# Kernel tuning notes

Measured on AMD Instinct MI355X. Metric: run time of the kernel, lower is better.

The kernel has to match this reference:

```python
import jax, jax.numpy as jnp
import numpy as np

N = 8192
IN_F = 512
OUT_F = 128
ALPHA = 0.2  # leaky relu negative slope
NEG_BIG = -1e10
RND_SCALE = 1e5


def setup_inputs() -> dict:
    key = jax.random.key(0)
    k1, k2, k3, k4, k5 = jax.random.split(key, 5)
    h = jax.random.normal(k1, (N, IN_F), dtype=jnp.float32)
    adj = jax.random.randint(k2, (N, N), 0, 2, dtype=jnp.int32)
    W = jax.random.normal(k3, (IN_F, OUT_F), dtype=jnp.float32) * 0.05
    a = jax.random.normal(k4, (2 * OUT_F, 1), dtype=jnp.float32) * 0.1
    # rnd in original is 1e5*(rand-0.5); same distribution here
    rnd = RND_SCALE * (jax.random.uniform(k5, (N, OUT_F), dtype=jnp.float32) - 0.5)
    return {"h": h, "adj": adj, "W": W, "a": a, "rnd": rnd}


def reference(h, adj, W, a, rnd):
    Wh = h @ W                              # [N, OUT_F]
    Wh1 = Wh @ a[:OUT_F, :]                 # [N, 1]
    Wh2 = Wh @ a[OUT_F:, :]                 # [N, 1]
    e = jax.nn.leaky_relu(Wh1 + Wh2.T, negative_slope=ALPHA)  # [N, N]
    attention = jnp.where(adj > 0, e, NEG_BIG)
    attention = jax.nn.softmax(attention, axis=1)
    h_prime = attention @ Wh                # [N, OUT_F]
    h_prime = (h_prime + rnd) / RND_SCALE
    return jax.nn.elu(h_prime)
```

## Files before the change

kernel.cpp:

```cpp
#include <hip/hip_runtime.h>

#define N 8192
#define IN_F 512
#define OUT_F 128
#define NW (N / 8)
#define SPLITK 8
#define KC 1024
#define LOG2E 1.4426950408889634f
#define LN2 0.6931471805599453f

typedef __attribute__((ext_vector_type(4))) float f32x4;
typedef __attribute__((ext_vector_type(8))) short bf16x8;
typedef __attribute__((ext_vector_type(8))) unsigned short u16x8;

__device__ __forceinline__ short f2bf(float f) {
    union { float f; unsigned u; } c; c.f = f;
    unsigned r = c.u + 0x7FFFu + ((c.u >> 16) & 1u);
    return (short)(r >> 16);
}

__device__ __forceinline__ float exp2fast(float x) {
#if __has_builtin(__builtin_amdgcn_exp2f)
    return __builtin_amdgcn_exp2f(x);
#else
    return __expf(x * LN2);
#endif
}

__device__ __forceinline__ void load_lds16(const void* g, void* l) {
    __builtin_amdgcn_global_load_lds((const __attribute__((address_space(1))) unsigned*)g,
                                     (__attribute__((address_space(3))) unsigned*)l,
                                     16, 0, 0);
}

__global__ __launch_bounds__(256) void conv_W(const float* __restrict__ W, short* __restrict__ WT) {
    int idx = blockIdx.x * 256 + threadIdx.x;
    int n = idx & (OUT_F - 1);
    int k = idx >> 7;
    WT[(size_t)n * IN_F + k] = f2bf(W[idx]);
}

__global__ __launch_bounds__(256) void mkmask(const int* __restrict__ adj,
                                              unsigned char* __restrict__ maskR) {
    const int wave = threadIdx.x >> 6, lane = threadIdx.x & 63;
    const size_t m = (size_t)blockIdx.x * 4 + wave;
    const int4* ap = (const int4*)(adj + m * N);
    unsigned char* mp = maskR + m * NW;
#pragma unroll 4
    for (int it = 0; it < 16; it++) {
        int b4 = it * 128 + lane * 2;
        int4 a0 = ap[b4], a1 = ap[b4 + 1];
        unsigned b = (unsigned)(a0.x > 0) | ((unsigned)(a0.y > 0) << 1) |
                     ((unsigned)(a0.z > 0) << 2) | ((unsigned)(a0.w > 0) << 3) |
                     ((unsigned)(a1.x > 0) << 4) | ((unsigned)(a1.y > 0) << 5) |
                     ((unsigned)(a1.z > 0) << 6) | ((unsigned)(a1.w > 0) << 7);
        mp[it * 64 + lane] = (unsigned char)b;
    }
}

__global__ __launch_bounds__(256) void gemm_hW(const float* __restrict__ h,
                                               const short* __restrict__ WT,
                                               const float* __restrict__ a,
                                               short* __restrict__ WhT,
                                               float* __restrict__ sOut,
                                               float* __restrict__ tOut) {
    const int tid = threadIdx.x;
    const int wave = tid >> 6, lane = tid & 63;
    const int row16 = lane & 15, kgrp = lane >> 4;
    const int m0 = blockIdx.x * 16;
    const int kbase = wave * 128;

    f32x4 acc[8] = {};
    const float4* hp = (const float4*)(h + (size_t)(m0 + row16) * IN_F + kbase);

#pragma unroll
    for (int kk = 0; kk < 128; kk += 32) {
        float4 u0 = hp[kk / 4 + kgrp * 2];
        float4 u1 = hp[kk / 4 + kgrp * 2 + 1];
        bf16x8 af;
        af[0] = f2bf(u0.x); af[1] = f2bf(u0.y); af[2] = f2bf(u0.z); af[3] = f2bf(u0.w);
        af[4] = f2bf(u1.x); af[5] = f2bf(u1.y); af[6] = f2bf(u1.z); af[7] = f2bf(u1.w);
#pragma unroll
        for (int nt = 0; nt < 8; nt++) {
            bf16x8 bf_ = *(const bf16x8*)(WT + (size_t)(nt * 16 + row16) * IN_F + kbase + kk + kgrp * 8);
            acc[nt] = __builtin_amdgcn_mfma_f32_16x16x32_bf16(af, bf_, acc[nt], 0, 0, 0);
        }
    }

    __shared__ float red[4][16][132];
#pragma unroll
    for (int nt = 0; nt < 8; nt++)
#pragma unroll
        for (int r = 0; r < 4; r++)
            red[wave][kgrp * 4 + r][nt * 16 + row16] = acc[nt][r];
    __syncthreads();

    const int row = tid >> 4, seg = tid & 15;
    float v[8];
#pragma unroll
    for (int e = 0; e < 8; e++) {
        int c = seg * 8 + e;
        v[e] = red[0][row][c] + red[1][row][c] + red[2][row][c] + red[3][row][c];
    }
    float sp = 0.f, tp = 0.f;
#pragma unroll
    for (int e = 0; e < 8; e++) {
        sp += v[e] * a[seg * 8 + e];
        tp += v[e] * a[OUT_F + seg * 8 + e];
    }
    sp += __shfl_xor(sp, 1); tp += __shfl_xor(tp, 1);
    sp += __shfl_xor(sp, 2); tp += __shfl_xor(tp, 2);
    sp += __shfl_xor(sp, 4); tp += __shfl_xor(tp, 4);
    sp += __shfl_xor(sp, 8); tp += __shfl_xor(tp, 8);
    if (seg == 0) {
        sOut[m0 + row] = sp * LOG2E;
        tOut[m0 + row] = tp * LOG2E;
    }
#pragma unroll
    for (int e = 0; e < 8; e++)
        WhT[(size_t)(seg * 8 + e) * N + m0 + row] = f2bf(v[e]);
}

__global__ __launch_bounds__(256, 4) void attn(const unsigned char* __restrict__ maskR,
                                               const short* __restrict__ WhT,
                                               const float* __restrict__ s,
                                               const float* __restrict__ t,
                                               unsigned short* __restrict__ num,
                                               float* __restrict__ lpart) {
    const int tid = threadIdx.x;
    const int wave = tid >> 6, lane = tid & 63;
    const int row16 = lane & 15, kgrp = lane >> 4;
    const int m0 = blockIdx.x * 64 + wave * 16;
    const int m  = m0 + row16;
    const int ks = blockIdx.y * KC;

    __shared__ short Bs[2][2][128 * 32];
    __shared__ float tl[KC];

    for (int i = tid; i < KC; i += 256) tl[i] = t[ks + i];

    const float s_m = s[m];
    const int4* mp = (const int4*)(maskR + (size_t)m * NW + (ks >> 3));
    int4 mcur = mp[0], mnxt = mp[1];

    auto stageB = [&](int sup, int par) {
        const int k0 = ks + sup * 64;
#pragma unroll
        for (int d = 0; d < 2; d++)
#pragma unroll
            for (int q = 0; q < 2; q++) {
                int nrow = wave * 32 + q * 16 + (lane >> 2);
                const short* g = WhT + (size_t)nrow * N + k0 + d * 32 + (lane & 3) * 8;
                load_lds16(g, &Bs[par][d][(wave * 32 + q * 16) * 32]);
            }
    };

    f32x4 acc[8] = {};
    float lsum = 0.f;

    stageB(0, 0);
    __syncthreads();

    for (int sp2 = 0; sp2 < 8; sp2++) {
#pragma unroll
        for (int ss = 0; ss < 2; ss++) {
            const int sp = sp2 * 2 + ss;
            const int par = sp & 1;
            if (sp + 1 < 16) stageB(sp + 1, par ^ 1);
#pragma unroll
            for (int d = 0; d < 2; d++) {
                const int g = sp * 2 + d;
                const unsigned dw = (unsigned)((const int*)&mcur)[ss * 2 + d];
                const unsigned mbyte = (dw >> (kgrp * 8)) & 0xFFu;

                const float* tp = tl + g * 32 + kgrp * 8;
                float4 tA = *(const float4*)tp;
                float4 tB = *(const float4*)(tp + 4);
                float tv[8] = { tA.x, tA.y, tA.z, tA.w, tB.x, tB.y, tB.z, tB.w };

                bf16x8 bfr[8];
                const short* base = &Bs[par][d][0];
#pragma unroll
                for (int ni = 0; ni < 8; ni++)
                    bfr[ni] = *(const bf16x8*)(base + (ni * 16 + row16) * 32 + kgrp * 8);

                unsigned pu[8];
#pragma unroll
                for (int e = 0; e < 8; e++) {
                    float x = s_m + tv[e];
                    x = fmaxf(x, 0.2f * x);
                    float p = exp2fast(x);
                    unsigned u = __float_as_uint(p) & 0xFFFF0000u;
                    u = ((mbyte >> e) & 1u) ? u : 0u;
                    lsum += __uint_as_float(u);
                    pu[e] = u;
                }
                bf16x8 af;
                unsigned* au = (unsigned*)&af;
#pragma unroll
                for (int q = 0; q < 4; q++) au[q] = (pu[2 * q] >> 16) | pu[2 * q + 1];
#pragma unroll
                for (int ni = 0; ni < 8; ni++)
                    acc[ni] = __builtin_amdgcn_mfma_f32_16x16x32_bf16(af, bfr[ni], acc[ni], 0, 0, 0);
            }
            __syncthreads();
        }
        mcur = mnxt;
        if (sp2 + 2 < 8) mnxt = mp[sp2 + 2];
    }

    {
        float v = lsum;
        v += __shfl_xor(v, 16);
        v += __shfl_xor(v, 32);
        if (kgrp == 0) lpart[(size_t)blockIdx.y * N + m] = v;
    }

    unsigned short* np_ = num + ((size_t)blockIdx.y * N + m0) * OUT_F;
#pragma unroll
    for (int ni = 0; ni < 8; ni++) {
        int n = ni * 16 + row16;
#pragma unroll
        for (int r = 0; r < 4; r++)
            np_[(size_t)(kgrp * 4 + r) * OUT_F + n] = (unsigned short)f2bf(acc[ni][r]);
    }
}

__global__ __launch_bounds__(256) void finalize(const unsigned short* __restrict__ num,
                                                const float* __restrict__ lpart,
                                                const float* __restrict__ rnd,
                                                float* __restrict__ out) {
    int idx = blockIdx.x * 256 + threadIdx.x;
    int m = idx >> 4;
    int c = (idx & 15) * 8;
    size_t g = (size_t)m * OUT_F + c;

    float nm[8] = {};
#pragma unroll
    for (int bk = 0; bk < SPLITK; bk++) {
        u16x8 v = *(const u16x8*)(num + (size_t)bk * N * OUT_F + g);
#pragma unroll
        for (int e = 0; e < 8; e++) nm[e] += __uint_as_float((unsigned)v[e] << 16);
    }
    float l = 0.f;
#pragma unroll
    for (int bk = 0; bk < SPLITK; bk++) l += lpart[(size_t)bk * N + m];
    float inv = 1.f / fmaxf(l, 1e-30f);

    float4 r0 = *(const float4*)(rnd + g);
    float4 r1 = *(const float4*)(rnd + g + 4);
    float rv[8] = { r0.x, r0.y, r0.z, r0.w, r1.x, r1.y, r1.z, r1.w };
    float ov[8];
#pragma unroll
    for (int e = 0; e < 8; e++) {
        float x = (nm[e] * inv + rv[e]) * 1e-5f;
        ov[e] = x > 0.f ? x : __expf(x) - 1.f;
    }
    *(float4*)(out + g)     = make_float4(ov[0], ov[1], ov[2], ov[3]);
    *(float4*)(out + g + 4) = make_float4(ov[4], ov[5], ov[6], ov[7]);
}

extern "C" void kernel_launch(void* const* d_in, const int* in_sizes, int n_in,
                              void* d_out, int out_size, void* d_ws, size_t ws_size,
                              hipStream_t stream) {
    const float* h   = (const float*)d_in[0];
    const int*   adj = (const int*)d_in[1];
    const float* W   = (const float*)d_in[2];
    const float* a   = (const float*)d_in[3];
    const float* rnd = (const float*)d_in[4];
    float* out = (float*)d_out;

    char* w = (char*)d_ws;
    short* WT    = (short*)(w);
    short* WhT   = (short*)(w + 131072);
    float* sv    = (float*)(w + 2228224);
    float* tv    = (float*)(w + 2260992);
    float* lpart = (float*)(w + 2293760);
    unsigned char* maskR = (unsigned char*)(w + 2555904);
    unsigned short* num  = (unsigned short*)(w + 10944512);

    conv_W  <<<256, 256, 0, stream>>>(W, WT);
    mkmask  <<<2048, 256, 0, stream>>>(adj, maskR);
    gemm_hW <<<512, 256, 0, stream>>>(h, WT, a, WhT, sv, tv);
    attn    <<<dim3(128, SPLITK), 256, 0, stream>>>(maskR, WhT, sv, tv, num, lpart);
    finalize<<<(N * OUT_F / 8) / 256, 256, 0, stream>>>(num, lpart, rnd, out);
}
```

Before: 427.3 us.

## Fuse adjacency mask construction into attention kernel, dropping separate bitmask pass

The separate mkmask kernel is removed. The attention kernel now streams int32 adjacency tiles straight from global memory into registers, prefetched one step ahead, and converts them to byte masks in per-wave LDS. Each lane then reads its 8 mask bytes as a 64-bit word. The t vector is read from global memory each step instead of being cached in LDS. This avoids the extra kernel launch and the maskR write and re-read. In exchange the attn kernel carries the full 256MB adjacency read inside its main loop, which adds register and memory pressure there.

Result: slower. 437.8 us (+2.4%).

```diff
diff --git a/kernel.cpp b/kernel.cpp
--- a/kernel.cpp
+++ b/kernel.cpp
@@ -3,7 +3,6 @@
 #define N 8192
 #define IN_F 512
 #define OUT_F 128
-#define NW (N / 8)
 #define SPLITK 8
 #define KC 1024
 #define LOG2E 1.4426950408889634f
@@ -38,24 +37,6 @@
     int n = idx & (OUT_F - 1);
     int k = idx >> 7;
     WT[(size_t)n * IN_F + k] = f2bf(W[idx]);
-}
-
-__global__ __launch_bounds__(256) void mkmask(const int* __restrict__ adj,
-                                              unsigned char* __restrict__ maskR) {
-    const int wave = threadIdx.x >> 6, lane = threadIdx.x & 63;
-    const size_t m = (size_t)blockIdx.x * 4 + wave;
-    const int4* ap = (const int4*)(adj + m * N);
-    unsigned char* mp = maskR + m * NW;
-#pragma unroll 4
-    for (int it = 0; it < 16; it++) {
-        int b4 = it * 128 + lane * 2;
-        int4 a0 = ap[b4], a1 = ap[b4 + 1];
-        unsigned b = (unsigned)(a0.x > 0) | ((unsigned)(a0.y > 0) << 1) |
-                     ((unsigned)(a0.z > 0) << 2) | ((unsigned)(a0.w > 0) << 3) |
-                     ((unsigned)(a1.x > 0) << 4) | ((unsigned)(a1.y > 0) << 5) |
-                     ((unsigned)(a1.z > 0) << 6) | ((unsigned)(a1.w > 0) << 7);
-        mp[it * 64 + lane] = (unsigned char)b;
-    }
 }
 
 __global__ __launch_bounds__(256) void gemm_hW(const float* __restrict__ h,
@@ -121,7 +102,7 @@
         WhT[(size_t)(seg * 8 + e) * N + m0 + row] = f2bf(v[e]);
 }
 
-__global__ __launch_bounds__(256, 4) void attn(const unsigned char* __restrict__ maskR,
+__global__ __launch_bounds__(256, 4) void attn(const int* __restrict__ adj,
                                                const short* __restrict__ WhT,
                                                const float* __restrict__ s,
                                                const float* __restrict__ t,
@@ -130,18 +111,19 @@
     const int tid = threadIdx.x;
     const int wave = tid >> 6, lane = tid & 63;
     const int row16 = lane & 15, kgrp = lane >> 4;
-    const int m0 = blockIdx.x * 64 + wave * 16;
-    const int m  = m0 + row16;
+    const int m0 = blockIdx.x * 64;
+    const int mw = m0 + wave * 16;
+    const int m  = mw + row16;
     const int ks = blockIdx.y * KC;
 
     __shared__ short Bs[2][2][128 * 32];
-    __shared__ float tl[KC];
-
-    for (int i = tid; i < KC; i += 256) tl[i] = t[ks + i];
-
+    __shared__ unsigned char amask[4][16 * 64];
+
+    unsigned char* amW = amask[wave];
     const float s_m = s[m];
-    const int4* mp = (const int4*)(maskR + (size_t)m * NW + (ks >> 3));
-    int4 mcur = mp[0], mnxt = mp[1];
+
+    const int ldrow = lane >> 4;
+    const int kq = (lane & 15) * 4;
 
     auto stageB = [&](int sup, int par) {
         const int k0 = ks + sup * 64;
@@ -158,55 +140,70 @@
     f32x4 acc[8] = {};
     float lsum = 0.f;
 
+    int4 G[4];
+#pragma unroll
+    for (int q = 0; q < 4; q++)
+        G[q] = *(const int4*)(adj + (size_t)(mw + q * 4 + ldrow) * N + ks + kq);
     stageB(0, 0);
     __syncthreads();
 
-    for (int sp2 = 0; sp2 < 8; sp2++) {
-#pragma unroll
-        for (int ss = 0; ss < 2; ss++) {
-            const int sp = sp2 * 2 + ss;
-            const int par = sp & 1;
-            if (sp + 1 < 16) stageB(sp + 1, par ^ 1);
-#pragma unroll
-            for (int d = 0; d < 2; d++) {
-                const int g = sp * 2 + d;
-                const unsigned dw = (unsigned)((const int*)&mcur)[ss * 2 + d];
-                const unsigned mbyte = (dw >> (kgrp * 8)) & 0xFFu;
-
-                const float* tp = tl + g * 32 + kgrp * 8;
-                float4 tA = *(const float4*)tp;
-                float4 tB = *(const float4*)(tp + 4);
-                float tv[8] = { tA.x, tA.y, tA.z, tA.w, tB.x, tB.y, tB.z, tB.w };
-
-                bf16x8 bfr[8];
-                const short* base = &Bs[par][d][0];
-#pragma unroll
-                for (int ni = 0; ni < 8; ni++)
-                    bfr[ni] = *(const bf16x8*)(base + (ni * 16 + row16) * 32 + kgrp * 8);
-
-                unsigned pu[8];
-#pragma unroll
-                for (int e = 0; e < 8; e++) {
-                    float x = s_m + tv[e];
-                    x = fmaxf(x, 0.2f * x);
-                    float p = exp2fast(x);
-                    unsigned u = __float_as_uint(p) & 0xFFFF0000u;
-                    u = ((mbyte >> e) & 1u) ? u : 0u;
-                    lsum += __uint_as_float(u);
-                    pu[e] = u;
-                }
-                bf16x8 af;
-                unsigned* au = (unsigned*)&af;
-#pragma unroll
-                for (int q = 0; q < 4; q++) au[q] = (pu[2 * q] >> 16) | pu[2 * q + 1];
-#pragma unroll
-                for (int ni = 0; ni < 8; ni++)
-                    acc[ni] = __builtin_amdgcn_mfma_f32_16x16x32_bf16(af, bfr[ni], acc[ni], 0, 0, 0);
+    for (int sp = 0; sp < 16; sp++) {
+        const int par = sp & 1;
+
+        const float* tb = t + ks + sp * 64 + kgrp * 8;
+        float4 t0a = *(const float4*)tb;
+        float4 t0b = *(const float4*)(tb + 4);
+        float4 t1a = *(const float4*)(tb + 32);
+        float4 t1b = *(const float4*)(tb + 36);
+
+#pragma unroll
+        for (int q = 0; q < 4; q++) {
+            int4 v = G[q];
+            unsigned dw = (v.x > 0 ? 0x1u : 0u) | (v.y > 0 ? 0x100u : 0u) |
+                          (v.z > 0 ? 0x10000u : 0u) | (v.w > 0 ? 0x1000000u : 0u);
+            *(unsigned*)(amW + (q * 4 + ldrow) * 64 + kq) = dw;
+        }
+        if (sp + 1 < 16) {
+#pragma unroll
+            for (int q = 0; q < 4; q++)
+                G[q] = *(const int4*)(adj + (size_t)(mw + q * 4 + ldrow) * N + ks + (sp + 1) * 64 + kq);
+            stageB(sp + 1, par ^ 1);
+        }
+
+#pragma unroll
+        for (int d = 0; d < 2; d++) {
+            float4 ta = d ? t1a : t0a;
+            float4 tb2 = d ? t1b : t0b;
+            float tv[8] = { ta.x, ta.y, ta.z, ta.w, tb2.x, tb2.y, tb2.z, tb2.w };
+
+            unsigned long long mk = *(const unsigned long long*)(amW + row16 * 64 + d * 32 + kgrp * 8);
+
+            bf16x8 bfr[8];
+            const short* base = &Bs[par][d][0];
+#pragma unroll
+            for (int ni = 0; ni < 8; ni++)
+                bfr[ni] = *(const bf16x8*)(base + (ni * 16 + row16) * 32 + kgrp * 8);
+
+            unsigned pu[8];
+#pragma unroll
+            for (int e = 0; e < 8; e++) {
+                float x = s_m + tv[e];
+                x = fmaxf(x, 0.2f * x);
+                float p = exp2fast(x);
+                unsigned u = __float_as_uint(p) & 0xFFFF0000u;
+                u = ((unsigned)(mk >> (8 * e)) & 1u) ? u : 0u;
+                lsum += __uint_as_float(u);
+                pu[e] = u;
             }
-            __syncthreads();
-        }
-        mcur = mnxt;
-        if (sp2 + 2 < 8) mnxt = mp[sp2 + 2];
+            bf16x8 af;
+            unsigned* au = (unsigned*)&af;
+#pragma unroll
+            for (int q = 0; q < 4; q++) au[q] = (pu[2 * q] >> 16) | pu[2 * q + 1];
+#pragma unroll
+            for (int ni = 0; ni < 8; ni++)
+                acc[ni] = __builtin_amdgcn_mfma_f32_16x16x32_bf16(af, bfr[ni], acc[ni], 0, 0, 0);
+        }
+        __syncthreads();
     }
 
     {
@@ -216,7 +213,7 @@
         if (kgrp == 0) lpart[(size_t)blockIdx.y * N + m] = v;
     }
 
-    unsigned short* np_ = num + ((size_t)blockIdx.y * N + m0) * OUT_F;
+    unsigned short* np_ = num + ((size_t)blockIdx.y * N + mw) * OUT_F;
 #pragma unroll
     for (int ni = 0; ni < 8; ni++) {
         int n = ni * 16 + row16;
@@ -276,12 +273,10 @@
     float* sv    = (float*)(w + 2228224);
     float* tv    = (float*)(w + 2260992);
     float* lpart = (float*)(w + 2293760);
-    unsigned char* maskR = (unsigned char*)(w + 2555904);
-    unsigned short* num  = (unsigned short*)(w + 10944512);
+    unsigned short* num = (unsigned short*)(w + 2555904);
 
     conv_W  <<<256, 256, 0, stream>>>(W, WT);
-    mkmask  <<<2048, 256, 0, stream>>>(adj, maskR);
     gemm_hW <<<512, 256, 0, stream>>>(h, WT, a, WhT, sv, tv);
-    attn    <<<dim3(128, SPLITK), 256, 0, stream>>>(maskR, WhT, sv, tv, num, lpart);
+    attn    <<<dim3(128, SPLITK), 256, 0, stream>>>(adj, WhT, sv, tv, num, lpart);
     finalize<<<(N * OUT_F / 8) / 256, 256, 0, stream>>>(num, lpart, rnd, out);
 }
```
